# Kernel tuning notes

Measured on AMD Instinct MI355X. Metric: run time of the kernel, lower is better.

Reference implementation:

```python
import jax, jax.numpy as jnp
import numpy as np

ENC_DIM = 256
DEC_DIM = 256
INT_DIM = 256


def setup_inputs() -> dict:
    key = jax.random.key(0)
    k1, k2, k3, k4, k5 = jax.random.split(key, 5)
    B, T = 64, 2048
    encoder_states = jax.random.normal(k1, (B, T, ENC_DIM), dtype=jnp.float32)
    decoder_state = jax.random.normal(k2, (B, DEC_DIM), dtype=jnp.float32)
    s1 = 1.0 / np.sqrt(ENC_DIM)
    s2 = 1.0 / np.sqrt(DEC_DIM)
    s3 = 1.0 / np.sqrt(INT_DIM)
    w1 = jax.random.uniform(k3, (INT_DIM, ENC_DIM), jnp.float32, -s1, s1)
    w2 = jax.random.uniform(k4, (INT_DIM, DEC_DIM), jnp.float32, -s2, s2)
    v = jax.random.uniform(k5, (1, INT_DIM), jnp.float32, -s3, s3)
    return {"encoder_states": encoder_states, "decoder_state": decoder_state,
            "w1": w1, "w2": w2, "v": v}


def reference(encoder_states, decoder_state, w1, w2, v):
    # scores: v @ tanh(W1 e_t + W2 d) for all t at once
    enc_proj = jnp.einsum('bte,ie->bti', encoder_states, w1)      # [B,T,I]
    dec_proj = jnp.einsum('bd,id->bi', decoder_state, w2)          # [B,I]
    scores = jnp.einsum('bti,oi->bt', jnp.tanh(enc_proj + dec_proj[:, None, :]), v)  # [B,T]
    attention_probs = jax.nn.softmax(scores, axis=1)[:, :, None]   # [B,T,1]
    final_context_vec = jnp.sum(attention_probs * encoder_states, axis=1)  # [B,E]
    return final_context_vec, attention_probs
```

## Files before the change

### kernel.cpp

```cpp
#include <hip/hip_runtime.h>
#include <hip/hip_bf16.h>
#include <math.h>

#define Bq 64
#define Tq 2048
#define Eq 256
#define Dq 256
#define Iq 256

using short8  = __attribute__((ext_vector_type(8))) short;
using floatx4 = __attribute__((ext_vector_type(4))) float;

__device__ __forceinline__ float fast_tanh(float x) {
    float e = __expf(2.0f * x);
    return 1.0f - 2.0f / (e + 1.0f);
}

__device__ __forceinline__ ushort f2bf(float x) {
    union { __hip_bfloat16 h; ushort u; } c;
    c.h = __float2bfloat16(x);
    return c.u;
}

__global__ __launch_bounds__(256) void prep_kernel(
    const float* __restrict__ w1, ushort* __restrict__ w1sw,
    const float* __restrict__ dec, const float* __restrict__ w2,
    float* __restrict__ dproj)
{
    if (blockIdx.x < 32) {
        const int kc = blockIdx.x;
        const int i  = threadIdx.x;
        const float* src = w1 + i * Eq + kc * 8;
        float4 f0 = *(const float4*)src;
        float4 f1 = *(const float4*)(src + 4);
        ushort u[8] = { f2bf(f0.x), f2bf(f0.y), f2bf(f0.z), f2bf(f0.w),
                        f2bf(f1.x), f2bf(f1.y), f2bf(f1.z), f2bf(f1.w) };
        *(short8*)&w1sw[(kc * 256 + i) * 8] = *(short8*)u;
    } else {
        const int b = blockIdx.x - 32;
        const int i = threadIdx.x;
        __shared__ float dls[Dq];
        dls[i] = dec[b * Dq + i];
        __syncthreads();
        const float* w2r = w2 + i * Dq;
        float acc = 0.f;
        #pragma unroll 8
        for (int d = 0; d < Dq; ++d) acc += dls[d] * w2r[d];
        dproj[b * Iq + i] = acc;
    }
}

__global__ __launch_bounds__(256, 3) void scores_ctx_kernel(
    const float*  __restrict__ enc,
    const ushort* __restrict__ w1sw,
    const float*  __restrict__ v,
    const float*  __restrict__ dproj,
    float* __restrict__ escore,
    float* __restrict__ ctxp,
    float* __restrict__ denomp)
{
    const int b   = blockIdx.y;
    const int bx  = blockIdx.x;
    const int t0  = bx * 64;
    const int tid = threadIdx.x;
    const int w   = tid >> 6;
    const int l   = tid & 63;
    const int l15 = l & 15;
    const int lq  = l >> 4;
    const int iBase = w * 64 + l15;

    __shared__ float red2[256 * 20];
    ushort* As = (ushort*)red2;
    __shared__ float vls[Iq], dls[Iq];
    __shared__ float pv[64];

    vls[tid] = v[tid];
    dls[tid] = dproj[b * Iq + tid];

    floatx4 acc[4][4];
    #pragma unroll
    for (int mi = 0; mi < 4; ++mi)
        #pragma unroll
        for (int ni = 0; ni < 4; ++ni)
            acc[mi][ni] = (floatx4)0.f;

    const float* encB = enc + ((size_t)b * Tq + t0) * Eq;
    const int rowp = tid >> 4;
    const int c4   = (tid & 15) * 4;

    float4 pre[4];
    #pragma unroll
    for (int r = 0; r < 4; ++r)
        pre[r] = *(const float4*)&encB[(rowp + 16 * r) * Eq + c4];

    #pragma unroll
    for (int kb = 0; kb < 4; ++kb) {
        ushort* Asp = As + (kb & 1) * (64 * 72);
        #pragma unroll
        for (int r = 0; r < 4; ++r) {
            ushort4 u;
            u.x = f2bf(pre[r].x); u.y = f2bf(pre[r].y);
            u.z = f2bf(pre[r].z); u.w = f2bf(pre[r].w);
            *(ushort4*)&Asp[(rowp + 16 * r) * 72 + c4] = u;
        }
        __syncthreads();
        if (kb < 3) {
            #pragma unroll
            for (int r = 0; r < 4; ++r)
                pre[r] = *(const float4*)&encB[(rowp + 16 * r) * Eq + (kb + 1) * 64 + c4];
        }
        #pragma unroll
        for (int ks = 0; ks < 2; ++ks) {
            const int kc = kb * 8 + ks * 4 + lq;
            short8 bfv[4], af[4];
            #pragma unroll
            for (int ni = 0; ni < 4; ++ni)
                bfv[ni] = *(const short8*)&w1sw[((size_t)kc * 256 + iBase + ni * 16) * 8];
            #pragma unroll
            for (int mi = 0; mi < 4; ++mi)
                af[mi] = *(const short8*)&Asp[(mi * 16 + l15) * 72 + ks * 32 + lq * 8];
            #pragma unroll
            for (int mi = 0; mi < 4; ++mi)
                #pragma unroll
                for (int ni = 0; ni < 4; ++ni)
                    acc[mi][ni] = __builtin_amdgcn_mfma_f32_16x16x32_bf16(
                        af[mi], bfv[ni], acc[mi][ni], 0, 0, 0);
        }
    }

    float part[4][4];
    #pragma unroll
    for (int mi = 0; mi < 4; ++mi)
        #pragma unroll
        for (int r = 0; r < 4; ++r) part[mi][r] = 0.f;

    #pragma unroll
    for (int ni = 0; ni < 4; ++ni) {
        const int i   = w * 64 + ni * 16 + l15;
        const float vi = vls[i];
        const float dp = dls[i];
        #pragma unroll
        for (int mi = 0; mi < 4; ++mi)
            #pragma unroll
            for (int r = 0; r < 4; ++r)
                part[mi][r] += vi * fast_tanh(acc[mi][ni][r] + dp);
    }

    __syncthreads();

    #pragma unroll
    for (int mi = 0; mi < 4; ++mi)
        #pragma unroll
        for (int r = 0; r < 4; ++r)
            red2[(w * 64 + mi * 16 + lq * 4 + r) * 20 + l15] = part[mi][r];
    __syncthreads();

    if (tid < 64) {
        float s = 0.f;
        #pragma unroll
        for (int ww = 0; ww < 4; ++ww) {
            const float* rp = red2 + (ww * 64 + tid) * 20;
            float4 q0 = *(const float4*)(rp + 0);
            float4 q1 = *(const float4*)(rp + 4);
            float4 q2 = *(const float4*)(rp + 8);
            float4 q3 = *(const float4*)(rp + 12);
            s += (q0.x + q0.y + q0.z + q0.w) + (q1.x + q1.y + q1.z + q1.w)
               + (q2.x + q2.y + q2.z + q2.w) + (q3.x + q3.y + q3.z + q3.w);
        }
        const float es = __expf(s);
        pv[tid] = es;
        escore[(size_t)b * Tq + t0 + tid] = es;
        float tot = es;
        tot += __shfl_xor(tot, 1);  tot += __shfl_xor(tot, 2);
        tot += __shfl_xor(tot, 4);  tot += __shfl_xor(tot, 8);
        tot += __shfl_xor(tot, 16); tot += __shfl_xor(tot, 32);
        if (tid == 0) denomp[bx * Bq + b] = tot;
    }
    __syncthreads();

    const int tg = tid >> 6;
    const int el = (tid & 63) * 4;
    float4 a = {0.f, 0.f, 0.f, 0.f};
    #pragma unroll 4
    for (int tt = 0; tt < 16; ++tt) {
        const int t = tg * 16 + tt;
        const float pt = pv[t];
        float4 ev = *(const float4*)&encB[t * Eq + el];
        a.x += pt * ev.x; a.y += pt * ev.y; a.z += pt * ev.z; a.w += pt * ev.w;
    }
    float* redf = red2;
    *(float4*)&redf[tg * 256 + el] = a;
    __syncthreads();
    if (tg == 0) {
        float4 a0 = *(const float4*)&redf[0 * 256 + el];
        float4 a1 = *(const float4*)&redf[1 * 256 + el];
        float4 a2 = *(const float4*)&redf[2 * 256 + el];
        float4 a3 = *(const float4*)&redf[3 * 256 + el];
        float4 o;
        o.x = a0.x + a1.x + a2.x + a3.x;
        o.y = a0.y + a1.y + a2.y + a3.y;
        o.z = a0.z + a1.z + a2.z + a3.z;
        o.w = a0.w + a1.w + a2.w + a3.w;
        *(float4*)&ctxp[((size_t)bx * Bq + b) * Eq + el] = o;
    }
}

__global__ __launch_bounds__(256) void finalize_kernel(
    const float* __restrict__ ctxp, const float* __restrict__ denomp,
    float* __restrict__ probs, float* __restrict__ ctx)
{
    const int b   = blockIdx.x;
    const int tid = threadIdx.x;

    float d = denomp[(tid & 31) * Bq + b];
    d += __shfl_xor(d, 1);  d += __shfl_xor(d, 2);  d += __shfl_xor(d, 4);
    d += __shfl_xor(d, 8);  d += __shfl_xor(d, 16);
    const float inv = 1.0f / d;

    float* prow = probs + (size_t)b * Tq + tid * 8;
    float4 p0 = *(const float4*)(prow + 0);
    float4 p1 = *(const float4*)(prow + 4);
    p0.x *= inv; p0.y *= inv; p0.z *= inv; p0.w *= inv;
    p1.x *= inv; p1.y *= inv; p1.z *= inv; p1.w *= inv;
    *(float4*)(prow + 0) = p0;
    *(float4*)(prow + 4) = p1;

    float s = 0.f;
    #pragma unroll 8
    for (int c = 0; c < 32; ++c)
        s += ctxp[((size_t)c * Bq + b) * Eq + tid];
    ctx[b * Eq + tid] = s * inv;
}

extern "C" void kernel_launch(void* const* d_in, const int* in_sizes, int n_in,
                              void* d_out, int out_size, void* d_ws, size_t ws_size,
                              hipStream_t stream) {
    const float* enc = (const float*)d_in[0];
    const float* dec = (const float*)d_in[1];
    const float* w1  = (const float*)d_in[2];
    const float* w2  = (const float*)d_in[3];
    const float* v   = (const float*)d_in[4];

    float* out   = (float*)d_out;
    float* ctx   = out;
    float* probs = out + Bq * Eq;

    char* ws = (char*)d_ws;
    float*  ctxp   = (float*)ws;
    float*  denomp = (float*)(ws + (32*Bq*Eq)*4);
    float*  dproj  = (float*)(ws + (32*Bq*Eq)*4 + 32*Bq*4);
    ushort* w1sw   = (ushort*)(ws + (32*Bq*Eq)*4 + 32*Bq*4 + Bq*Iq*4);

    prep_kernel<<<dim3(96), dim3(256), 0, stream>>>(w1, w1sw, dec, w2, dproj);
    scores_ctx_kernel<<<dim3(Tq / 64, Bq), dim3(256), 0, stream>>>(
        enc, w1sw, v, dproj, probs, ctxp, denomp);
    finalize_kernel<<<dim3(Bq), dim3(256), 0, stream>>>(ctxp, denomp, probs, ctx);
}
```

Baseline: 234.5 us.

## Stage full encoder tile in LDS once and prefetch W1 fragments across k-steps

Replaces the four-stage double-buffered K loop with a single upfront load of the whole 64x256 encoder tile into LDS as bf16, issued as two batches of 8 row loads, followed by one barrier. The MFMA loop then runs eight k-steps without barriers and register-prefetches the next W1 fragments while computing the current ones. This removes three barriers and the per-stage conversion interleaving. The cost is more shared memory (about 33KB for the tile), which may lower occupancy, and the global-load latency is no longer overlapped with the MFMA work.

```diff
diff --git a/kernel.cpp b/kernel.cpp
--- a/kernel.cpp
+++ b/kernel.cpp
@@ -69,8 +69,7 @@
     const int lq  = l >> 4;
     const int iBase = w * 64 + l15;
 
-    __shared__ float red2[256 * 20];
-    ushort* As = (ushort*)red2;
+    __shared__ ushort As[64 * 264];
     __shared__ float vls[Iq], dls[Iq];
     __shared__ float pv[64];
 
@@ -85,47 +84,55 @@
             acc[mi][ni] = (floatx4)0.f;
 
     const float* encB = enc + ((size_t)b * Tq + t0) * Eq;
-    const int rowp = tid >> 4;
-    const int c4   = (tid & 15) * 4;
-
-    float4 pre[4];
-    #pragma unroll
-    for (int r = 0; r < 4; ++r)
-        pre[r] = *(const float4*)&encB[(rowp + 16 * r) * Eq + c4];
-
-    #pragma unroll
-    for (int kb = 0; kb < 4; ++kb) {
-        ushort* Asp = As + (kb & 1) * (64 * 72);
-        #pragma unroll
-        for (int r = 0; r < 4; ++r) {
-            ushort4 u;
-            u.x = f2bf(pre[r].x); u.y = f2bf(pre[r].y);
-            u.z = f2bf(pre[r].z); u.w = f2bf(pre[r].w);
-            *(ushort4*)&Asp[(rowp + 16 * r) * 72 + c4] = u;
-        }
-        __syncthreads();
-        if (kb < 3) {
-            #pragma unroll
-            for (int r = 0; r < 4; ++r)
-                pre[r] = *(const float4*)&encB[(rowp + 16 * r) * Eq + (kb + 1) * 64 + c4];
-        }
-        #pragma unroll
-        for (int ks = 0; ks < 2; ++ks) {
-            const int kc = kb * 8 + ks * 4 + lq;
-            short8 bfv[4], af[4];
+    const int lane4 = l * 4;
+
+    float4 pre[8];
+    #pragma unroll
+    for (int j = 0; j < 8; ++j)
+        pre[j] = *(const float4*)&encB[(j * 4 + w) * Eq + lane4];
+    #pragma unroll
+    for (int j = 0; j < 8; ++j) {
+        ushort4 u;
+        u.x = f2bf(pre[j].x); u.y = f2bf(pre[j].y);
+        u.z = f2bf(pre[j].z); u.w = f2bf(pre[j].w);
+        *(ushort4*)&As[(j * 4 + w) * 264 + lane4] = u;
+    }
+    #pragma unroll
+    for (int j = 8; j < 16; ++j)
+        pre[j - 8] = *(const float4*)&encB[(j * 4 + w) * Eq + lane4];
+    #pragma unroll
+    for (int j = 8; j < 16; ++j) {
+        ushort4 u;
+        u.x = f2bf(pre[j - 8].x); u.y = f2bf(pre[j - 8].y);
+        u.z = f2bf(pre[j - 8].z); u.w = f2bf(pre[j - 8].w);
+        *(ushort4*)&As[(j * 4 + w) * 264 + lane4] = u;
+    }
+    __syncthreads();
+
+    short8 bcur[4], bnext[4];
+    #pragma unroll
+    for (int ni = 0; ni < 4; ++ni)
+        bcur[ni] = *(const short8*)&w1sw[((size_t)lq * 256 + iBase + ni * 16) * 8];
+    #pragma unroll
+    for (int kstep = 0; kstep < 8; ++kstep) {
+        if (kstep < 7) {
+            const int kc = (kstep + 1) * 4 + lq;
             #pragma unroll
             for (int ni = 0; ni < 4; ++ni)
-                bfv[ni] = *(const short8*)&w1sw[((size_t)kc * 256 + iBase + ni * 16) * 8];
+                bnext[ni] = *(const short8*)&w1sw[((size_t)kc * 256 + iBase + ni * 16) * 8];
+        }
+        short8 af[4];
+        #pragma unroll
+        for (int mi = 0; mi < 4; ++mi)
+            af[mi] = *(const short8*)&As[(mi * 16 + l15) * 264 + kstep * 32 + lq * 8];
+        #pragma unroll
+        for (int mi = 0; mi < 4; ++mi)
             #pragma unroll
-            for (int mi = 0; mi < 4; ++mi)
-                af[mi] = *(const short8*)&Asp[(mi * 16 + l15) * 72 + ks * 32 + lq * 8];
-            #pragma unroll
-            for (int mi = 0; mi < 4; ++mi)
-                #pragma unroll
-                for (int ni = 0; ni < 4; ++ni)
-                    acc[mi][ni] = __builtin_amdgcn_mfma_f32_16x16x32_bf16(
-                        af[mi], bfv[ni], acc[mi][ni], 0, 0, 0);
-        }
+            for (int ni = 0; ni < 4; ++ni)
+                acc[mi][ni] = __builtin_amdgcn_mfma_f32_16x16x32_bf16(
+                    af[mi], bcur[ni], acc[mi][ni], 0, 0, 0);
+        #pragma unroll
+        for (int ni = 0; ni < 4; ++ni) bcur[ni] = bnext[ni];
     }
 
     float part[4][4];
@@ -148,6 +155,7 @@
 
     __syncthreads();
 
+    float* red2 = (float*)As;
     #pragma unroll
     for (int mi = 0; mi < 4; ++mi)
         #pragma unroll
@@ -188,7 +196,7 @@
         float4 ev = *(const float4*)&encB[t * Eq + el];
         a.x += pt * ev.x; a.y += pt * ev.y; a.z += pt * ev.z; a.w += pt * ev.w;
     }
-    float* redf = red2;
+    float* redf = (float*)As;
     *(float4*)&redf[tg * 256 + el] = a;
     __syncthreads();
     if (tg == 0) {
```

Result: no change. 233.9 us (-0.2%).
